# Kernel tuning notes

Hardware: AMD Instinct MI355X
Metric: run time of the kernel (lower is better)

## Reference

```python
import jax, jax.numpy as jnp
import numpy as np

WS = (4, 4, 4)      # window size (d, h, w)
SS = (2, 2, 2)      # shift size
NH = 12             # num heads
EPS = 1e-5


def _rel_pos_index(ws):
    # static numpy, identical to the torch buffer construction
    coords = np.stack(np.meshgrid(np.arange(ws[0]), np.arange(ws[1]), np.arange(ws[2]), indexing='ij'))
    cf = coords.reshape(3, -1)                       # (3, N)
    rc = cf[:, :, None] - cf[:, None, :]             # (3, N, N)
    rc = rc.transpose(1, 2, 0).astype(np.int64)      # (N, N, 3)
    rc[..., 0] += ws[0] - 1
    rc[..., 1] += ws[1] - 1
    rc[..., 2] += ws[2] - 1
    rc[..., 0] *= (2 * ws[1] - 1) * (2 * ws[2] - 1)
    rc[..., 1] *= 2 * ws[2] - 1
    return rc.sum(-1)                                # (N, N)


def _attn_mask(Dp, Hp, Wp, ws, ss):
    # static numpy mask for shifted windows: (nW, N, N), 0 or -100
    img = np.zeros((Dp, Hp, Wp))
    sl = lambda w, s: (slice(0, -w), slice(-w, -s), slice(-s, None))
    cnt = 0
    for d in sl(ws[0], ss[0]):
        for h in sl(ws[1], ss[1]):
            for w in sl(ws[2], ss[2]):
                img[d, h, w] = cnt
                cnt += 1
    m = img.reshape(Dp // ws[0], ws[0], Hp // ws[1], ws[1], Wp // ws[2], ws[2])
    m = m.transpose(0, 2, 4, 1, 3, 5).reshape(-1, ws[0] * ws[1] * ws[2])  # (nW, N)
    am = m[:, None, :] - m[:, :, None]
    return np.where(am != 0, -100.0, 0.0).astype(np.float32)


def _window_partition(x, ws):
    B, D, H, W, C = x.shape
    x = x.reshape(B, D // ws[0], ws[0], H // ws[1], ws[1], W // ws[2], ws[2], C)
    return x.transpose(0, 1, 3, 5, 2, 4, 6, 7).reshape(-1, ws[0] * ws[1] * ws[2], C)


def _window_reverse(win, ws, B, D, H, W):
    C = win.shape[-1]
    x = win.reshape(B, D // ws[0], H // ws[1], W // ws[2], ws[0], ws[1], ws[2], C)
    return x.transpose(0, 1, 4, 2, 5, 3, 6, 7).reshape(B, D, H, W, C)


def _layernorm(x, g, b):
    mu = jnp.mean(x, axis=-1, keepdims=True)
    var = jnp.mean(jnp.square(x - mu), axis=-1, keepdims=True)
    return (x - mu) * jax.lax.rsqrt(var + EPS) * g + b


def setup_inputs() -> dict:
    key = jax.random.key(0)
    ks = jax.random.split(key, 8)
    C, HID = 384, 1536
    s = 0.02
    return {
        'x': jax.random.normal(ks[0], (2, 16, 56, 56, C), jnp.float32),
        'norm1_g': jnp.ones((C,), jnp.float32),
        'norm1_b': jnp.zeros((C,), jnp.float32),
        'qkv_w': jax.random.normal(ks[1], (C, 3 * C), jnp.float32) * s,
        'qkv_b': jnp.zeros((3 * C,), jnp.float32),
        'rpb_table': jax.random.normal(ks[2], (343, NH), jnp.float32) * s,
        'proj_w': jax.random.normal(ks[3], (C, C), jnp.float32) * s,
        'proj_b': jnp.zeros((C,), jnp.float32),
        'norm2_g': jnp.ones((C,), jnp.float32),
        'norm2_b': jnp.zeros((C,), jnp.float32),
        'fc1_w': jax.random.normal(ks[4], (C, HID), jnp.float32) * s,
        'fc1_b': jnp.zeros((HID,), jnp.float32),
        'fc2_w': jax.random.normal(ks[5], (HID, C), jnp.float32) * s,
        'fc2_b': jnp.zeros((C,), jnp.float32),
    }


def reference(x, norm1_g, norm1_b, qkv_w, qkv_b, rpb_table, proj_w, proj_b,
              norm2_g, norm2_b, fc1_w, fc1_b, fc2_w, fc2_b):
    B, D, H, W, C = x.shape
    N = WS[0] * WS[1] * WS[2]
    hd = C // NH
    scale = hd ** -0.5

    shortcut = x
    h = _layernorm(x, norm1_g, norm1_b)
    # dims are divisible by window; pad amounts are zero (torch pad path is a no-op)
    Dp, Hp, Wp = D, H, W

    shifted = jnp.roll(h, shift=(-SS[0], -SS[1], -SS[2]), axis=(1, 2, 3))
    win = _window_partition(shifted, WS)                 # (B*nW, N, C)
    Bw = win.shape[0]
    nW = Bw // B

    qkv = (win @ qkv_w + qkv_b).reshape(Bw, N, 3, NH, hd)
    q, k, v = qkv[:, :, 0], qkv[:, :, 1], qkv[:, :, 2]   # (Bw, N, NH, hd)
    attn = jnp.einsum('bnhd,bmhd->bhnm', q * scale, k)   # (Bw, NH, N, N)

    rel_idx = jnp.asarray(_rel_pos_index(WS))            # (N, N) static
    bias = rpb_table[rel_idx.reshape(-1)].reshape(N, N, NH).transpose(2, 0, 1)
    attn = attn + bias[None]

    mask = jnp.asarray(_attn_mask(Dp, Hp, Wp, WS, SS))   # (nW, N, N) static
    attn = attn.reshape(B, nW, NH, N, N) + mask[None, :, None]
    attn = jax.nn.softmax(attn.reshape(Bw, NH, N, N), axis=-1)

    out = jnp.einsum('bhnm,bmhd->bnhd', attn, v).reshape(Bw, N, C)
    out = out @ proj_w + proj_b

    shifted = _window_reverse(out, WS, B, Dp, Hp, Wp)
    h = jnp.roll(shifted, shift=(SS[0], SS[1], SS[2]), axis=(1, 2, 3))

    x = shortcut + h
    h2 = _layernorm(x, norm2_g, norm2_b)
    h2 = jax.nn.gelu(h2 @ fc1_w + fc1_b, approximate=False) @ fc2_w + fc2_b
    return x + h2
```

## Files before the change

kernel.cpp:

```cpp
#include <hip/hip_runtime.h>
#include <math.h>

typedef unsigned short u16;
typedef float v4f __attribute__((ext_vector_type(4)));
typedef short v8s __attribute__((ext_vector_type(8)));

__device__ __forceinline__ u16 f2bf(float f) {
  union { float f; unsigned u; } c; c.f = f;
  unsigned u = c.u;
  u += 0x7fff + ((u >> 16) & 1);
  return (u16)(u >> 16);
}

__device__ __forceinline__ int row_to_token(int r) {
  int win = r >> 6, n = r & 63;
  int b = (win >= 784) ? 1 : 0;
  int wrem = win - b * 784;
  int wd = wrem / 196;
  int r2 = wrem - wd * 196;
  int wh = r2 / 14;
  int ww = r2 - wh * 14;
  int d = wd * 4 + (n >> 4);
  int h = wh * 4 + ((n >> 2) & 3);
  int w = ww * 4 + (n & 3);
  d = (d + 2) & 15;
  h += 2; if (h >= 56) h -= 56;
  w += 2; if (w >= 56) w -= 56;
  return ((b * 16 + d) * 56 + h) * 56 + w;
}

__device__ __forceinline__ int region_label(int n, int bd, int bh, int bw) {
  int ld = bd ? (((n >> 4) >= 2) ? 2 : 1) : 0;
  int lh = bh ? ((((n >> 2) & 3) >= 2) ? 2 : 1) : 0;
  int lw = bw ? (((n & 3) >= 2) ? 2 : 1) : 0;
  return ld * 9 + lh * 3 + lw;
}

__global__ __launch_bounds__(256) void transpose_w(const float* __restrict__ src, u16* __restrict__ dst,
                                                   int K, int N) {
  __shared__ u16 t[32][33];
  int kt = blockIdx.x * 32, nt = blockIdx.y * 32;
  int lx = threadIdx.x & 31, ly = threadIdx.x >> 5;
#pragma unroll
  for (int i = 0; i < 32; i += 8)
    t[ly + i][lx] = f2bf(src[(size_t)(kt + ly + i) * N + nt + lx]);
  __syncthreads();
#pragma unroll
  for (int i = 0; i < 32; i += 8)
    dst[(size_t)(nt + ly + i) * K + kt + lx] = t[lx][ly + i];
}

__global__ __launch_bounds__(256) void bias_kernel(const float* __restrict__ rpb, float* __restrict__ biasb) {
  int i = blockIdx.x * 256 + threadIdx.x;
  int h = i >> 12, n = (i >> 6) & 63, m = i & 63;
  int dd = (n >> 4) - (m >> 4) + 3;
  int dh = ((n >> 2) & 3) - ((m >> 2) & 3) + 3;
  int dw = (n & 3) - (m & 3) + 3;
  biasb[i] = rpb[(dd * 49 + dh * 7 + dw) * 12 + h];
}

template<bool MAP>
__global__ __launch_bounds__(256) void ln_kernel(const float* __restrict__ x, const float* __restrict__ g,
                                                 const float* __restrict__ bta, u16* __restrict__ out) {
  int wid = threadIdx.x >> 6, lane = threadIdx.x & 63;
  int r = blockIdx.x * 4 + wid;
  int t = MAP ? row_to_token(r) : r;
  const float* src = x + (size_t)t * 384;
  float v[6]; float s = 0.f;
#pragma unroll
  for (int i = 0; i < 6; i++) { v[i] = src[lane + i * 64]; s += v[i]; }
#pragma unroll
  for (int off = 1; off < 64; off <<= 1) s += __shfl_xor(s, off);
  float mu = s * (1.f / 384.f);
  float vs = 0.f;
#pragma unroll
  for (int i = 0; i < 6; i++) { float d = v[i] - mu; vs += d * d; }
#pragma unroll
  for (int off = 1; off < 64; off <<= 1) vs += __shfl_xor(vs, off);
  float rstd = 1.f / sqrtf(vs * (1.f / 384.f) + 1e-5f);
  u16* dst = out + (size_t)r * 384;
#pragma unroll
  for (int i = 0; i < 6; i++) {
    int c = lane + i * 64;
    dst[c] = f2bf((v[i] - mu) * rstd * g[c] + bta[c]);
  }
}

template<int EPI>
__global__ __launch_bounds__(256) void gemm_bf16(const u16* __restrict__ A, const u16* __restrict__ Bw,
                                                 const float* __restrict__ bias, int M, int N, int K,
                                                 u16* __restrict__ out_bf, float* __restrict__ out_f,
                                                 const float* __restrict__ resid) {
  __shared__ u16 As[128][40];
  __shared__ u16 Bs[128][40];
  const int tid = threadIdx.x;
  const int n0 = blockIdx.x * 128;
  const int m0 = blockIdx.y * 128;
  const int wid = tid >> 6, lane = tid & 63;
  const int wm = (wid >> 1) * 64, wn = (wid & 1) * 64;
  const int l15 = lane & 15, q4 = lane >> 4;
  v4f acc[4][4];
#pragma unroll
  for (int i = 0; i < 4; i++)
#pragma unroll
    for (int j = 0; j < 4; j++) acc[i][j] = (v4f){0.f, 0.f, 0.f, 0.f};

  const int srow = tid >> 2, skc = (tid & 3) * 8;

  for (int k0 = 0; k0 < K; k0 += 32) {
#pragma unroll
    for (int i = 0; i < 2; i++) {
      int r = srow + i * 64;
      float4 ld = *(const float4*)(A + (size_t)(m0 + r) * K + k0 + skc);
      *(float4*)&As[r][skc] = ld;
    }
#pragma unroll
    for (int i = 0; i < 2; i++) {
      int r = srow + i * 64;
      float4 ld = *(const float4*)(Bw + (size_t)(n0 + r) * K + k0 + skc);
      *(float4*)&Bs[r][skc] = ld;
    }
    __syncthreads();
    v8s afr[4], bfr[4];
#pragma unroll
    for (int tm = 0; tm < 4; tm++) afr[tm] = *(const v8s*)&As[wm + tm * 16 + l15][q4 * 8];
#pragma unroll
    for (int tn = 0; tn < 4; tn++) bfr[tn] = *(const v8s*)&Bs[wn + tn * 16 + l15][q4 * 8];
#pragma unroll
    for (int tm = 0; tm < 4; tm++)
#pragma unroll
      for (int tn = 0; tn < 4; tn++)
        acc[tm][tn] = __builtin_amdgcn_mfma_f32_16x16x32_bf16(afr[tm], bfr[tn], acc[tm][tn], 0, 0, 0);
    __syncthreads();
  }

#pragma unroll
  for (int tm = 0; tm < 4; tm++) {
#pragma unroll
    for (int tn = 0; tn < 4; tn++) {
      const int gcol = n0 + wn + tn * 16 + l15;
      const float bb = bias[gcol];
#pragma unroll
      for (int r = 0; r < 4; r++) {
        const int grow = m0 + wm + tm * 16 + q4 * 4 + r;
        float val = acc[tm][tn][r] + bb;
        if constexpr (EPI == 0) {
          out_bf[(size_t)grow * N + gcol] = f2bf(val);
        } else if constexpr (EPI == 2) {
          val = 0.5f * val * (1.f + erff(val * 0.70710678118654752f));
          out_bf[(size_t)grow * N + gcol] = f2bf(val);
        } else if constexpr (EPI == 1) {
          int t_ = row_to_token(grow);
          out_f[(size_t)t_ * 384 + gcol] = resid[(size_t)t_ * 384 + gcol] + val;
        } else {
          out_f[(size_t)grow * 384 + gcol] += val;
        }
      }
    }
  }
}

__global__ __launch_bounds__(256) void attn_kernel(const u16* __restrict__ qkv, const float* __restrict__ biasb,
                                                   u16* __restrict__ outb) {
  __shared__ u16 P[4][64][72];
  int wid = threadIdx.x >> 6, lane = threadIdx.x & 63;
  int g = blockIdx.x * 4 + wid;
  int win = g / 12, head = g - win * 12;
  int l15 = lane & 15, q4 = lane >> 4;
  const u16* base = qkv + (size_t)win * 64 * 1152;
  const u16* qp = base + head * 32;
  const u16* kp = base + 384 + head * 32;
  const u16* vp = base + 768 + head * 32;

  v8s a[4], kb[4];
#pragma unroll
  for (int tm = 0; tm < 4; tm++) a[tm] = *(const v8s*)(qp + (size_t)(tm * 16 + l15) * 1152 + q4 * 8);
#pragma unroll
  for (int tn = 0; tn < 4; tn++) kb[tn] = *(const v8s*)(kp + (size_t)(tn * 16 + l15) * 1152 + q4 * 8);
  v4f acc[4][4];
#pragma unroll
  for (int i = 0; i < 4; i++)
#pragma unroll
    for (int j = 0; j < 4; j++) acc[i][j] = (v4f){0.f, 0.f, 0.f, 0.f};
#pragma unroll
  for (int tm = 0; tm < 4; tm++)
#pragma unroll
    for (int tn = 0; tn < 4; tn++)
      acc[tm][tn] = __builtin_amdgcn_mfma_f32_16x16x32_bf16(a[tm], kb[tn], acc[tm][tn], 0, 0, 0);

  int wrem = win % 784;
  int wd = wrem / 196, r2 = wrem % 196, wh = r2 / 14, ww = r2 % 14;
  int bd = (wd == 3), bh = (wh == 13), bw = (ww == 13);
  const float* bptr = biasb + head * 4096;
  int mlab[4];
#pragma unroll
  for (int tn = 0; tn < 4; tn++) mlab[tn] = region_label(tn * 16 + l15, bd, bh, bw);

#pragma unroll
  for (int tm = 0; tm < 4; tm++) {
#pragma unroll
    for (int r = 0; r < 4; r++) {
      int n = tm * 16 + q4 * 4 + r;
      int nlab = region_label(n, bd, bh, bw);
      float sv[4];
      float mx = -1e30f;
#pragma unroll
      for (int tn = 0; tn < 4; tn++) {
        int m = tn * 16 + l15;
        float s = acc[tm][tn][r] * 0.17677669529663687f + bptr[n * 64 + m];
        if (mlab[tn] != nlab) s -= 100.f;
        sv[tn] = s;
        mx = fmaxf(mx, s);
      }
#pragma unroll
      for (int off = 1; off < 16; off <<= 1) mx = fmaxf(mx, __shfl_xor(mx, off));
      float sum = 0.f;
#pragma unroll
      for (int tn = 0; tn < 4; tn++) { float e = __expf(sv[tn] - mx); sv[tn] = e; sum += e; }
#pragma unroll
      for (int off = 1; off < 16; off <<= 1) sum += __shfl_xor(sum, off);
      float inv = 1.f / sum;
#pragma unroll
      for (int tn = 0; tn < 4; tn++) P[wid][n][tn * 16 + l15] = f2bf(sv[tn] * inv);
    }
  }
  __syncthreads();

  v4f o[4][2];
#pragma unroll
  for (int i = 0; i < 4; i++) { o[i][0] = (v4f){0.f,0.f,0.f,0.f}; o[i][1] = (v4f){0.f,0.f,0.f,0.f}; }
#pragma unroll
  for (int kt = 0; kt < 2; kt++) {
    v8s pa[4];
#pragma unroll
    for (int tm = 0; tm < 4; tm++) pa[tm] = *(const v8s*)&P[wid][tm * 16 + l15][kt * 32 + q4 * 8];
#pragma unroll
    for (int tn = 0; tn < 2; tn++) {
      v8s vb;
#pragma unroll
      for (int j = 0; j < 8; j++) vb[j] = (short)vp[(size_t)(kt * 32 + q4 * 8 + j) * 1152 + tn * 16 + l15];
#pragma unroll
      for (int tm = 0; tm < 4; tm++)
        o[tm][tn] = __builtin_amdgcn_mfma_f32_16x16x32_bf16(pa[tm], vb, o[tm][tn], 0, 0, 0);
    }
  }
#pragma unroll
  for (int tm = 0; tm < 4; tm++)
#pragma unroll
    for (int tn = 0; tn < 2; tn++)
#pragma unroll
      for (int r = 0; r < 4; r++) {
        int n = tm * 16 + q4 * 4 + r;
        outb[(size_t)(win * 64 + n) * 384 + head * 32 + tn * 16 + l15] = f2bf(o[tm][tn][r]);
      }
}

extern "C" void kernel_launch(void* const* d_in, const int* in_sizes, int n_in,
                              void* d_out, int out_size, void* d_ws, size_t ws_size,
                              hipStream_t stream) {
  const float* x      = (const float*)d_in[0];
  const float* n1g    = (const float*)d_in[1];
  const float* n1b    = (const float*)d_in[2];
  const float* qkv_w  = (const float*)d_in[3];
  const float* qkv_b  = (const float*)d_in[4];
  const float* rpb    = (const float*)d_in[5];
  const float* proj_w = (const float*)d_in[6];
  const float* proj_b = (const float*)d_in[7];
  const float* n2g    = (const float*)d_in[8];
  const float* n2b    = (const float*)d_in[9];
  const float* fc1_w  = (const float*)d_in[10];
  const float* fc1_b  = (const float*)d_in[11];
  const float* fc2_w  = (const float*)d_in[12];
  const float* fc2_b  = (const float*)d_in[13];
  float* out = (float*)d_out;
  char* ws = (char*)d_ws;

  u16*   wb    = (u16*)ws;
  float* biasb = (float*)(ws + 3538944);
  u16*   lnbuf = (u16*)(ws + 3735552);
  u16*   qkvb  = (u16*)(ws + 80805888);
  u16*   attnb = (u16*)(ws + 312016896);
  u16*   fc1ob = (u16*)(ws + 80805888);

  u16* qkv_wt  = wb;
  u16* proj_wt = wb + 442368;
  u16* fc1_wt  = wb + 589824;
  u16* fc2_wt  = wb + 1179648;

  transpose_w<<<dim3(12, 36), 256, 0, stream>>>(qkv_w,  qkv_wt,  384, 1152);
  transpose_w<<<dim3(12, 12), 256, 0, stream>>>(proj_w, proj_wt, 384, 384);
  transpose_w<<<dim3(12, 48), 256, 0, stream>>>(fc1_w,  fc1_wt,  384, 1536);
  transpose_w<<<dim3(48, 12), 256, 0, stream>>>(fc2_w,  fc2_wt,  1536, 384);
  bias_kernel<<<192, 256, 0, stream>>>(rpb, biasb);
  ln_kernel<true><<<25088, 256, 0, stream>>>(x, n1g, n1b, lnbuf);
  gemm_bf16<0><<<dim3(9, 784), 256, 0, stream>>>(lnbuf, qkv_wt, qkv_b, 100352, 1152, 384, qkvb, nullptr, nullptr);
  attn_kernel<<<4704, 256, 0, stream>>>(qkvb, biasb, attnb);
  gemm_bf16<1><<<dim3(3, 784), 256, 0, stream>>>(attnb, proj_wt, proj_b, 100352, 384, 384, nullptr, out, x);
  ln_kernel<false><<<25088, 256, 0, stream>>>(out, n2g, n2b, lnbuf);
  gemm_bf16<2><<<dim3(12, 784), 256, 0, stream>>>(lnbuf, fc1_wt, fc1_b, 100352, 1536, 384, fc1ob, nullptr, nullptr);
  gemm_bf16<3><<<dim3(3, 784), 256, 0, stream>>>(fc1ob, fc2_wt, fc2_b, 100352, 384, 1536, nullptr, out, nullptr);
}
```

Measured before the change: 1.218 ms.

## Use direct global-to-LDS loads with XOR swizzle and XCD-aware block mapping in GEMM

The GEMM's A and B tiles are now staged with global_load_lds 16-byte transfers that write straight into LDS, replacing load-to-register then store. The LDS layout changes to an XOR swizzle to avoid bank conflicts, and the next tile's load is issued before the MFMAs so loading overlaps compute within a single buffer. The 2D grid becomes a 1D grid remapped so that blocks landing on the same XCD (bid&7) cover contiguous tiles, which should improve L2 reuse. The epilogue hoists bias loads and the row_to_token computation out of the inner loop.

```diff
diff --git a/kernel.cpp b/kernel.cpp
--- a/kernel.cpp
+++ b/kernel.cpp
@@ -10,6 +10,12 @@
   unsigned u = c.u;
   u += 0x7fff + ((u >> 16) & 1);
   return (u16)(u >> 16);
+}
+
+typedef __attribute__((address_space(1))) const unsigned int guint;
+typedef __attribute__((address_space(3))) unsigned int luint;
+__device__ __forceinline__ void gll16(const void* g, void* l) {
+  __builtin_amdgcn_global_load_lds((guint*)g, (luint*)l, 16, 0, 0);
 }
 
 __device__ __forceinline__ int row_to_token(int r) {
@@ -88,72 +94,99 @@
 
 template<int EPI>
 __global__ __launch_bounds__(256) void gemm_bf16(const u16* __restrict__ A, const u16* __restrict__ Bw,
-                                                 const float* __restrict__ bias, int M, int N, int K,
+                                                 const float* __restrict__ bias, int N, int K,
                                                  u16* __restrict__ out_bf, float* __restrict__ out_f,
-                                                 const float* __restrict__ resid) {
-  __shared__ u16 As[128][40];
-  __shared__ u16 Bs[128][40];
+                                                 const float* __restrict__ resid, int ntn) {
+  __shared__ __align__(16) u16 As[4096];
+  __shared__ __align__(16) u16 Bs[4096];
   const int tid = threadIdx.x;
-  const int n0 = blockIdx.x * 128;
-  const int m0 = blockIdx.y * 128;
+  const int nwg = gridDim.x;
+  const int bid = blockIdx.x;
+  const int swz = (bid & 7) * (nwg >> 3) + (bid >> 3);
+  const int by = swz / ntn;
+  const int bx = swz - by * ntn;
+  const int m0 = by * 128, n0 = bx * 128;
   const int wid = tid >> 6, lane = tid & 63;
   const int wm = (wid >> 1) * 64, wn = (wid & 1) * 64;
   const int l15 = lane & 15, q4 = lane >> 4;
+
+  const int u0 = tid, u1 = 256 + tid;
+  const int r0 = u0 >> 2, r1 = u1 >> 2;
+  const int c0 = ((u0 & 3) ^ ((r0 >> 1) & 3)) << 3;
+  const int c1 = ((u1 & 3) ^ ((r1 >> 1) & 3)) << 3;
+  const u16* ag0 = A + (size_t)(m0 + r0) * K + c0;
+  const u16* ag1 = A + (size_t)(m0 + r1) * K + c1;
+  const u16* bg0 = Bw + (size_t)(n0 + r0) * K + c0;
+  const u16* bg1 = Bw + (size_t)(n0 + r1) * K + c1;
+  u16* asd0 = As + (wid << 9);
+  u16* asd1 = As + 2048 + (wid << 9);
+  u16* bsd0 = Bs + (wid << 9);
+  u16* bsd1 = Bs + 2048 + (wid << 9);
+
+  int aoff[4], boff[4];
+#pragma unroll
+  for (int t = 0; t < 4; t++) {
+    int ra = wm + t * 16 + l15;
+    aoff[t] = ra * 64 + ((q4 ^ ((ra >> 1) & 3)) << 4);
+    int rb = wn + t * 16 + l15;
+    boff[t] = rb * 64 + ((q4 ^ ((rb >> 1) & 3)) << 4);
+  }
+
   v4f acc[4][4];
 #pragma unroll
   for (int i = 0; i < 4; i++)
 #pragma unroll
     for (int j = 0; j < 4; j++) acc[i][j] = (v4f){0.f, 0.f, 0.f, 0.f};
 
-  const int srow = tid >> 2, skc = (tid & 3) * 8;
-
-  for (int k0 = 0; k0 < K; k0 += 32) {
-#pragma unroll
-    for (int i = 0; i < 2; i++) {
-      int r = srow + i * 64;
-      float4 ld = *(const float4*)(A + (size_t)(m0 + r) * K + k0 + skc);
-      *(float4*)&As[r][skc] = ld;
-    }
-#pragma unroll
-    for (int i = 0; i < 2; i++) {
-      int r = srow + i * 64;
-      float4 ld = *(const float4*)(Bw + (size_t)(n0 + r) * K + k0 + skc);
-      *(float4*)&Bs[r][skc] = ld;
-    }
+  gll16(ag0, asd0); gll16(ag1, asd1);
+  gll16(bg0, bsd0); gll16(bg1, bsd1);
+  ag0 += 32; ag1 += 32; bg0 += 32; bg1 += 32;
+
+  const int nk = K >> 5;
+  for (int kk = 0; kk < nk; ++kk) {
     __syncthreads();
     v8s afr[4], bfr[4];
 #pragma unroll
-    for (int tm = 0; tm < 4; tm++) afr[tm] = *(const v8s*)&As[wm + tm * 16 + l15][q4 * 8];
-#pragma unroll
-    for (int tn = 0; tn < 4; tn++) bfr[tn] = *(const v8s*)&Bs[wn + tn * 16 + l15][q4 * 8];
+    for (int t = 0; t < 4; t++) {
+      afr[t] = *(const v8s*)((const char*)As + aoff[t]);
+      bfr[t] = *(const v8s*)((const char*)Bs + boff[t]);
+    }
+    __syncthreads();
+    if (kk + 1 < nk) {
+      gll16(ag0, asd0); gll16(ag1, asd1);
+      gll16(bg0, bsd0); gll16(bg1, bsd1);
+      ag0 += 32; ag1 += 32; bg0 += 32; bg1 += 32;
+    }
 #pragma unroll
     for (int tm = 0; tm < 4; tm++)
 #pragma unroll
       for (int tn = 0; tn < 4; tn++)
         acc[tm][tn] = __builtin_amdgcn_mfma_f32_16x16x32_bf16(afr[tm], bfr[tn], acc[tm][tn], 0, 0, 0);
-    __syncthreads();
-  }
-
+  }
+
+  float bb[4]; int gc[4];
+#pragma unroll
+  for (int tn = 0; tn < 4; tn++) { gc[tn] = n0 + wn + tn * 16 + l15; bb[tn] = bias[gc[tn]]; }
 #pragma unroll
   for (int tm = 0; tm < 4; tm++) {
 #pragma unroll
-    for (int tn = 0; tn < 4; tn++) {
-      const int gcol = n0 + wn + tn * 16 + l15;
-      const float bb = bias[gcol];
-#pragma unroll
-      for (int r = 0; r < 4; r++) {
-        const int grow = m0 + wm + tm * 16 + q4 * 4 + r;
-        float val = acc[tm][tn][r] + bb;
+    for (int r = 0; r < 4; r++) {
+      const int grow = m0 + wm + tm * 16 + q4 * 4 + r;
+      size_t rowbase;
+      if constexpr (EPI == 1) rowbase = (size_t)row_to_token(grow) * 384;
+      else rowbase = (size_t)grow * N;
+#pragma unroll
+      for (int tn = 0; tn < 4; tn++) {
+        float val = acc[tm][tn][r] + bb[tn];
         if constexpr (EPI == 0) {
-          out_bf[(size_t)grow * N + gcol] = f2bf(val);
+          out_bf[rowbase + gc[tn]] = f2bf(val);
         } else if constexpr (EPI == 2) {
           val = 0.5f * val * (1.f + erff(val * 0.70710678118654752f));
-          out_bf[(size_t)grow * N + gcol] = f2bf(val);
+          out_bf[rowbase + gc[tn]] = f2bf(val);
         } else if constexpr (EPI == 1) {
-          int t_ = row_to_token(grow);
-          out_f[(size_t)t_ * 384 + gcol] = resid[(size_t)t_ * 384 + gcol] + val;
+          out_f[rowbase + gc[tn]] = resid[rowbase + gc[tn]] + val;
         } else {
-          out_f[(size_t)grow * 384 + gcol] += val;
+          out_f[rowbase + gc[tn]] += val;
         }
       }
     }
@@ -293,10 +326,10 @@
   transpose_w<<<dim3(48, 12), 256, 0, stream>>>(fc2_w,  fc2_wt,  1536, 384);
   bias_kernel<<<192, 256, 0, stream>>>(rpb, biasb);
   ln_kernel<true><<<25088, 256, 0, stream>>>(x, n1g, n1b, lnbuf);
-  gemm_bf16<0><<<dim3(9, 784), 256, 0, stream>>>(lnbuf, qkv_wt, qkv_b, 100352, 1152, 384, qkvb, nullptr, nullptr);
+  gemm_bf16<0><<<dim3(9 * 784), 256, 0, stream>>>(lnbuf, qkv_wt, qkv_b, 1152, 384, qkvb, nullptr, nullptr, 9);
   attn_kernel<<<4704, 256, 0, stream>>>(qkvb, biasb, attnb);
-  gemm_bf16<1><<<dim3(3, 784), 256, 0, stream>>>(attnb, proj_wt, proj_b, 100352, 384, 384, nullptr, out, x);
+  gemm_bf16<1><<<dim3(3 * 784), 256, 0, stream>>>(attnb, proj_wt, proj_b, 384, 384, nullptr, out, x, 3);
   ln_kernel<false><<<25088, 256, 0, stream>>>(out, n2g, n2b, lnbuf);
-  gemm_bf16<2><<<dim3(12, 784), 256, 0, stream>>>(lnbuf, fc1_wt, fc1_b, 100352, 1536, 384, fc1ob, nullptr, nullptr);
-  gemm_bf16<3><<<dim3(3, 784), 256, 0, stream>>>(fc1ob, fc2_wt, fc2_b, 100352, 384, 1536, nullptr, out, nullptr);
-}
+  gemm_bf16<2><<<dim3(12 * 784), 256, 0, stream>>>(lnbuf, fc1_wt, fc1_b, 1536, 384, fc1ob, nullptr, nullptr, 12);
+  gemm_bf16<3><<<dim3(3 * 784), 256, 0, stream>>>(fc1ob, fc2_wt, fc2_b, 384, 1536, nullptr, out, nullptr, 3);
+}
```

New measurement: 1.112 ms. 8.7% less time.
